# Kernel optimization log

Hardware: AMD Instinct MI355X
Metric: run time of the kernel (lower is better)

The kernel has to match this reference:

```python
import jax, jax.numpy as jnp
import numpy as np

B, S, H = 2, 2048, 1024
NH, HD = 16, 64
SCALE = HD ** -0.5


def setup_inputs() -> dict:
    key = jax.random.key(0)
    k1, k2, k3, k4 = jax.random.split(key, 4)
    hidden_states = jax.random.normal(k1, (B, S, H), dtype=jnp.float32)
    attention_mask = jax.random.randint(k2, (B, S), 0, 2, dtype=jnp.int32)
    # xavier-uniform-ish init scale
    w_qkv = jax.random.normal(k3, (3 * H, H), dtype=jnp.float32) * (2.0 / (H + 3 * H)) ** 0.5
    w_out = jax.random.normal(k4, (H, H), dtype=jnp.float32) * (1.0 / H) ** 0.5
    return {"hidden_states": hidden_states, "attention_mask": attention_mask,
            "w_qkv": w_qkv, "w_out": w_out}


def reference(hidden_states, attention_mask, w_qkv, w_out):
    b, s, _ = hidden_states.shape
    qkv = hidden_states @ w_qkv.T                      # [B,S,3H]
    q, k, v = jnp.split(qkv, 3, axis=-1)
    # [B,S,H] -> [B,NH,S,HD]
    reshape = lambda x: x.reshape(b, s, NH, HD).transpose(0, 2, 1, 3)
    q, k, v = reshape(q), reshape(k), reshape(v)
    scores = jnp.einsum('bhqd,bhkd->bhqk', q, k) * SCALE   # [B,NH,S,S]
    mask = attention_mask[:, None, None, :] == 0           # [B,1,1,S]
    scores = jnp.where(mask, -jnp.inf, scores)
    attn = jax.nn.softmax(scores, axis=-1)                 # dropout p: eval mode -> identity
    out = jnp.einsum('bhqk,bhkd->bhqd', attn, v)           # [B,NH,S,HD]
    out = out.transpose(0, 2, 1, 3).reshape(b, s, H)
    return out @ w_out.T
```

## Files before the change

kernel.cpp:

```cpp
#include <hip/hip_runtime.h>
#include <string.h>


typedef __bf16    bf16x8 __attribute__((ext_vector_type(8)));
typedef _Float16  f16x4  __attribute__((ext_vector_type(4)));
typedef _Float16  f16x2  __attribute__((ext_vector_type(2)));
typedef float     f32x4  __attribute__((ext_vector_type(4)));

#define NTOK   4096
#define HDIM   1024
#define SEQ    2048
#define NHEAD  16
#define F2SHIFT 4.0f
#define QSCALE  0.18033688f
#define LSTRIDE 68

__device__ __forceinline__ float bf2f(unsigned short u) {
    union { unsigned int i; float f; } x;
    x.i = ((unsigned int)u) << 16;
    return x.f;
}
__device__ __forceinline__ unsigned short f2bf(float f) {
    union { __bf16 h; unsigned short u; } x;
    x.h = (__bf16)f;
    return x.u;
}
__device__ __forceinline__ unsigned short f2h(float f) {
    union { _Float16 h; unsigned short u; } x;
    x.h = (_Float16)f;
    return x.u;
}
__device__ __forceinline__ f16x2 pkrtz(float a, float b) {
    union { __fp16 __attribute__((ext_vector_type(2))) i; f16x2 o; } x;
    x.i = __builtin_amdgcn_cvt_pkrtz(a, b);
    return x.o;
}

__device__ __forceinline__ int detect_f32(const unsigned short* hs) {
    unsigned int idx = (threadIdx.x & 63) * 4096u;
    float f = bf2f(hs[idx]);
    return __any(!(fabsf(f) < 1e4f));
}

typedef const __attribute__((address_space(1))) unsigned int* gptr_u32;
typedef __attribute__((address_space(3))) unsigned int* lptr_u32;

__device__ __forceinline__ void async16(const unsigned short* g, unsigned short* l) {
    __builtin_amdgcn_global_load_lds((gptr_u32)g, (lptr_u32)l, 16, 0, 0);
}

__global__ void convert3_kernel(const void* __restrict__ s0, const void* __restrict__ s1,
                                const void* __restrict__ s2, unsigned short* __restrict__ dst) {
    const int isf32 = detect_f32((const unsigned short*)s0);
    if (!isf32) return;
    int g = blockIdx.x * blockDim.x + threadIdx.x;
    const int stride = gridDim.x * blockDim.x;
    for (; g < 1048576; g += stride) {
        int i = g * 8;
        const void* src; int off;
        if (i < 4194304)      { src = s0; off = i; }
        else if (i < 7340032) { src = s1; off = i - 4194304; }
        else                  { src = s2; off = i - 7340032; }
        const float* s = (const float*)src + off;
        unsigned short o[8];
#pragma unroll
        for (int j = 0; j < 8; j++) o[j] = f2bf(s[j]);
        *(uint4*)(dst + i) = *(const uint4*)o;
    }
}

__global__ __launch_bounds__(256) void gemm_qkv(
    const unsigned short* __restrict__ Xc, const unsigned short* __restrict__ Wc,
    const unsigned short* __restrict__ Xraw, const unsigned short* __restrict__ Wraw,
    unsigned short* __restrict__ q_out, unsigned short* __restrict__ k_out,
    unsigned short* __restrict__ v_out) {
    const int K = 1024;
    __shared__ __align__(16) unsigned short Xs[128 * 32];
    __shared__ __align__(16) unsigned short Ws[128 * 32];

    const int isf32 = detect_f32(Xraw);
    const unsigned short* X = isf32 ? Xc : Xraw;
    const unsigned short* W = isf32 ? Wc : Wraw;

    const int t = threadIdx.x;
    const int w = t >> 6, lane = t & 63, quad = lane >> 4, lr = lane & 15;
    const int wrow = (w >> 1) * 64, wcol = (w & 1) * 64;
    const int m0 = blockIdx.y * 128, n0 = blockIdx.x * 128;
    const bool vblk = (n0 >= 2048);

    f32x4 acc[4][4];
#pragma unroll
    for (int mi = 0; mi < 4; mi++)
#pragma unroll
        for (int ni = 0; ni < 4; ni++) acc[mi][ni] = (f32x4){0.f, 0.f, 0.f, 0.f};

    const int srow = w * 32 + (lane >> 2);
    const int scol = (lane & 3) * 8;
    const unsigned short* xg = X + (size_t)(m0 + srow) * K + scol;
    const unsigned short* wg = W + (size_t)(n0 + srow) * K + scol;
    unsigned short* xl0 = &Xs[w * 1024];
    unsigned short* wl0 = &Ws[w * 1024];

    for (int k0 = 0; k0 < K; k0 += 32) {
        __syncthreads();
        async16(xg + k0, xl0);
        async16(xg + k0 + 16 * K, xl0 + 512);
        async16(wg + k0, wl0);
        async16(wg + k0 + 16 * K, wl0 + 512);
        __syncthreads();
        bf16x8 af[4], bfr[4];
#pragma unroll
        for (int mi = 0; mi < 4; mi++)
            af[mi] = *(bf16x8*)&Xs[(wrow + mi * 16 + lr) * 32 + quad * 8];
#pragma unroll
        for (int ni = 0; ni < 4; ni++)
            bfr[ni] = *(bf16x8*)&Ws[(wcol + ni * 16 + lr) * 32 + quad * 8];
        if (!vblk) {
#pragma unroll
            for (int mi = 0; mi < 4; mi++)
#pragma unroll
                for (int ni = 0; ni < 4; ni++)
                    acc[mi][ni] = __builtin_amdgcn_mfma_f32_16x16x32_bf16(af[mi], bfr[ni], acc[mi][ni], 0, 0, 0);
        } else {
#pragma unroll
            for (int mi = 0; mi < 4; mi++)
#pragma unroll
                for (int ni = 0; ni < 4; ni++)
                    acc[mi][ni] = __builtin_amdgcn_mfma_f32_16x16x32_bf16(bfr[ni], af[mi], acc[mi][ni], 0, 0, 0);
        }
    }

    if (!vblk) {
#pragma unroll
        for (int mi = 0; mi < 4; mi++)
#pragma unroll
            for (int ni = 0; ni < 4; ni++)
#pragma unroll
                for (int rr = 0; rr < 4; rr++) {
                    int mrow = m0 + wrow + mi * 16 + quad * 4 + rr;
                    int j = n0 + wcol + ni * 16 + lr;
                    float val = acc[mi][ni][rr];
                    int which = j >> 10, rem = j & 1023;
                    int nh = rem >> 6, hd = rem & 63;
                    int b = mrow >> 11, s = mrow & 2047;
                    size_t dst = ((size_t)(b * NHEAD + nh) * SEQ + s) * 64 + hd;
                    if (which == 0) q_out[dst] = f2bf(val * QSCALE);
                    else            k_out[dst] = f2bf(val);
                }
    } else {
#pragma unroll
        for (int mi = 0; mi < 4; mi++)
#pragma unroll
            for (int ni = 0; ni < 4; ni++)
#pragma unroll
                for (int rr = 0; rr < 4; rr++) {
                    int n = n0 + wcol + ni * 16 + quad * 4 + rr;
                    int m = m0 + wrow + mi * 16 + lr;
                    float val = acc[mi][ni][rr];
                    int rem = n & 1023;
                    int nh = rem >> 6, hd = rem & 63;
                    int b = m >> 11, s = m & 2047;
                    size_t dst = ((size_t)(b * NHEAD + nh) * 64 + hd) * SEQ + s;
                    v_out[dst] = f2h(val);
                }
    }
}

__global__ __launch_bounds__(256) void gemm_out(
    const unsigned short* __restrict__ X, const unsigned short* __restrict__ Wc,
    const unsigned short* __restrict__ Wraw,
    void* __restrict__ d_out, const unsigned short* __restrict__ hs_raw) {
    const int K = 1024, N = 1024;
    __shared__ __align__(16) unsigned short Xs[64 * 32];
    __shared__ __align__(16) unsigned short Ws[128 * 32];

    const int isf32 = detect_f32(hs_raw);
    const unsigned short* W = isf32 ? Wc : Wraw;

    const int t = threadIdx.x;
    const int w = t >> 6, lane = t & 63, quad = lane >> 4, lr = lane & 15;
    const int wrow = (w >> 1) * 32, wcol = (w & 1) * 64;
    const int m0 = blockIdx.y * 64, n0 = blockIdx.x * 128;

    f32x4 acc[2][4];
#pragma unroll
    for (int mi = 0; mi < 2; mi++)
#pragma unroll
        for (int ni = 0; ni < 4; ni++) acc[mi][ni] = (f32x4){0.f, 0.f, 0.f, 0.f};

    const int sxrow = w * 16 + (lane >> 2);
    const int swrow = w * 32 + (lane >> 2);
    const int scol = (lane & 3) * 8;
    const unsigned short* xg = X + (size_t)(m0 + sxrow) * K + scol;
    const unsigned short* wg = W + (size_t)(n0 + swrow) * K + scol;
    unsigned short* xl0 = &Xs[w * 512];
    unsigned short* wl0 = &Ws[w * 1024];

    for (int k0 = 0; k0 < K; k0 += 32) {
        __syncthreads();
        async16(xg + k0, xl0);
        async16(wg + k0, wl0);
        async16(wg + k0 + 16 * K, wl0 + 512);
        __syncthreads();
        bf16x8 af[2], bfr[4];
#pragma unroll
        for (int mi = 0; mi < 2; mi++)
            af[mi] = *(bf16x8*)&Xs[(wrow + mi * 16 + lr) * 32 + quad * 8];
#pragma unroll
        for (int ni = 0; ni < 4; ni++)
            bfr[ni] = *(bf16x8*)&Ws[(wcol + ni * 16 + lr) * 32 + quad * 8];
#pragma unroll
        for (int mi = 0; mi < 2; mi++)
#pragma unroll
            for (int ni = 0; ni < 4; ni++)
                acc[mi][ni] = __builtin_amdgcn_mfma_f32_16x16x32_bf16(af[mi], bfr[ni], acc[mi][ni], 0, 0, 0);
    }

#pragma unroll
    for (int mi = 0; mi < 2; mi++)
#pragma unroll
        for (int ni = 0; ni < 4; ni++)
#pragma unroll
            for (int rr = 0; rr < 4; rr++) {
                int mrow = m0 + wrow + mi * 16 + quad * 4 + rr;
                int j = n0 + wcol + ni * 16 + lr;
                float val = acc[mi][ni][rr];
                size_t dst = (size_t)mrow * N + j;
                if (isf32) ((float*)d_out)[dst] = val;
                else ((unsigned short*)d_out)[dst] = f2bf(val);
            }
}

__global__ __launch_bounds__(256) void flash_attn_v8(
    const unsigned short* __restrict__ q, const unsigned short* __restrict__ k,
    const unsigned short* __restrict__ vt, const int* __restrict__ mask,
    unsigned short* __restrict__ attn_out) {
    __shared__ __align__(16) unsigned short Ks[2][64 * LSTRIDE];
    __shared__ __align__(16) unsigned short Vt[2][64 * LSTRIDE];
    __shared__ __align__(16) float Msk[2][80];

    const int t = threadIdx.x;
    const int w = t >> 6, lane = t & 63, quad = lane >> 4, lr = lane & 15;
    const int bh = blockIdx.x, b = bh >> 4, h = bh & 15;
    const int q0 = blockIdx.y * 128;

    const unsigned short* qb = q + (size_t)bh * SEQ * 64;
    const unsigned short* kb = k + (size_t)bh * SEQ * 64;
    const unsigned short* vtb = vt + (size_t)bh * 64 * SEQ;
    const int* mb = mask + b * SEQ;

    bf16x8 qf[2][2];
#pragma unroll
    for (int qg = 0; qg < 2; qg++) {
        const unsigned short* qrow = qb + (size_t)(q0 + w * 32 + qg * 16 + lr) * 64 + quad * 8;
        qf[qg][0] = *(const bf16x8*)qrow;
        qf[qg][1] = *(const bf16x8*)(qrow + 32);
    }

    f32x4 oacc[2][4];
#pragma unroll
    for (int qg = 0; qg < 2; qg++)
#pragma unroll
        for (int dt = 0; dt < 4; dt++) oacc[qg][dt] = (f32x4){0.f, 0.f, 0.f, 0.f};
    float l_st[2] = {0.f, 0.f};

    const int sr = t >> 2;
    const int sc = (t & 3) * 16;

    uint4 ka, kb2, va, vb2;
    float mval = 0.f;
    {
        const uint4* kp = (const uint4*)(kb + (size_t)sr * 64 + sc);
        const uint4* vp = (const uint4*)(vtb + (size_t)sr * SEQ + sc);
        ka = kp[0]; kb2 = kp[1];
        va = vp[0]; vb2 = vp[1];
        if (t < 64) mval = (mb[t] == 0) ? -1e30f : -F2SHIFT;
    }
    *(uint4*)&Ks[0][sr * LSTRIDE + sc] = ka;
    *(uint4*)&Ks[0][sr * LSTRIDE + sc + 8] = kb2;
    *(uint4*)&Vt[0][sr * LSTRIDE + sc] = va;
    *(uint4*)&Vt[0][sr * LSTRIDE + sc + 8] = vb2;
    if (t < 64) Msk[0][t] = mval;
    __syncthreads();

    int cur = 0;
    for (int kk0 = 0; kk0 < SEQ; kk0 += 64) {
        const int nxt = kk0 + 64;
        if (nxt < SEQ) {
            const uint4* kp = (const uint4*)(kb + (size_t)(nxt + sr) * 64 + sc);
            const uint4* vp = (const uint4*)(vtb + (size_t)sr * SEQ + nxt + sc);
            ka = kp[0]; kb2 = kp[1];
            va = vp[0]; vb2 = vp[1];
            if (t < 64) mval = (mb[nxt + t] == 0) ? -1e30f : -F2SHIFT;
        }

        __builtin_amdgcn_s_setprio(1);
#pragma unroll
        for (int mt = 0; mt < 4; mt++) {
            bf16x8 a1h0 = *(bf16x8*)&Ks[cur][(mt * 16 + lr) * LSTRIDE + quad * 8];
            bf16x8 a1h1 = *(bf16x8*)&Ks[cur][(mt * 16 + lr) * LSTRIDE + 32 + quad * 8];
            f16x4 a2[4];
#pragma unroll
            for (int dt = 0; dt < 4; dt++)
                a2[dt] = *(f16x4*)&Vt[cur][(dt * 16 + lr) * LSTRIDE + mt * 16 + quad * 4];
            float4 mv = *(const float4*)&Msk[cur][mt * 16 + quad * 4];
            f32x4 zi = (f32x4){mv.x, mv.y, mv.z, mv.w};

#pragma unroll
            for (int qg = 0; qg < 2; qg++) {
                f32x4 z = __builtin_amdgcn_mfma_f32_16x16x32_bf16(a1h0, qf[qg][0], zi, 0, 0, 0);
                z = __builtin_amdgcn_mfma_f32_16x16x32_bf16(a1h1, qf[qg][1], z, 0, 0, 0);
                float p0 = __builtin_amdgcn_exp2f(z[0]);
                float p1 = __builtin_amdgcn_exp2f(z[1]);
                float p2 = __builtin_amdgcn_exp2f(z[2]);
                float p3 = __builtin_amdgcn_exp2f(z[3]);
                l_st[qg] += (p0 + p1) + (p2 + p3);
                f16x2 ab = pkrtz(p0, p1);
                f16x2 cd = pkrtz(p2, p3);
                f16x4 b2;
                b2[0] = ab[0]; b2[1] = ab[1]; b2[2] = cd[0]; b2[3] = cd[1];
#pragma unroll
                for (int dt = 0; dt < 4; dt++)
                    oacc[qg][dt] = __builtin_amdgcn_mfma_f32_16x16x16f16(a2[dt], b2, oacc[qg][dt], 0, 0, 0);
            }
        }
        __builtin_amdgcn_s_setprio(0);

        if (nxt < SEQ) {
            __syncthreads();
            const int nb = cur ^ 1;
            *(uint4*)&Ks[nb][sr * LSTRIDE + sc] = ka;
            *(uint4*)&Ks[nb][sr * LSTRIDE + sc + 8] = kb2;
            *(uint4*)&Vt[nb][sr * LSTRIDE + sc] = va;
            *(uint4*)&Vt[nb][sr * LSTRIDE + sc + 8] = vb2;
            if (t < 64) Msk[nb][t] = mval;
            __syncthreads();
            cur = nb;
        }
    }

    float inv[2];
#pragma unroll
    for (int qg = 0; qg < 2; qg++) {
        float s = l_st[qg];
        s += __shfl_xor(s, 16);
        s += __shfl_xor(s, 32);
        inv[qg] = 1.0f / s;
    }
#pragma unroll
    for (int qg = 0; qg < 2; qg++) {
        size_t tok = (size_t)(b * SEQ + q0 + w * 32 + qg * 16 + lr);
#pragma unroll
        for (int dt = 0; dt < 4; dt++)
#pragma unroll
            for (int rr = 0; rr < 4; rr++)
                attn_out[tok * HDIM + h * 64 + dt * 16 + quad * 4 + rr] =
                    f2bf(oacc[qg][dt][rr] * inv[qg]);
    }
}

extern "C" void kernel_launch(void* const* d_in, const int* in_sizes, int n_in,
                              void* d_out, int out_size, void* d_ws, size_t ws_size,
                              hipStream_t stream) {
    const void* hs_raw = d_in[0];
    const int* mask = (const int*)d_in[1];
    const void* wqkv_raw = d_in[2];
    const void* wout_raw = d_in[3];

    char* wsb = (char*)d_ws;
    unsigned short* hs_c = (unsigned short*)(wsb + 256);
    unsigned short* wqkv_c = hs_c + 4194304;
    unsigned short* wout_c = wqkv_c + 3145728;
    unsigned short* qw = wout_c + 1048576;
    unsigned short* kw = qw + 4194304;
    unsigned short* vtw = kw + 4194304;
    unsigned short* ao = vtw + 4194304;

    convert3_kernel<<<1024, 256, 0, stream>>>(hs_raw, wqkv_raw, wout_raw, hs_c);

    gemm_qkv<<<dim3(24, 32), 256, 0, stream>>>(hs_c, wqkv_c,
                                               (const unsigned short*)hs_raw,
                                               (const unsigned short*)wqkv_raw,
                                               qw, kw, vtw);
    flash_attn_v8<<<dim3(32, 16), 256, 0, stream>>>(qw, kw, vtw, mask, ao);
    gemm_out<<<dim3(8, 64), 256, 0, stream>>>(ao, wout_c,
                                              (const unsigned short*)wout_raw, d_out,
                                              (const unsigned short*)hs_raw);
}
```

Measured before the change: 202.6 us.

## Split attention KV range across two warp groups per block and merge partials

The flash attention kernel now uses 512 threads, with two groups of 4 waves each covering half of the key sequence for the same 128 queries. Each group keeps its own double-buffered K/V/mask tiles in shared memory. At the end, group 1 writes its partial output accumulators and row sums to shared memory and group 0 adds them before normalising. This is meant to double the waves per block, adding latency hiding and parallelism for a grid of only 512 blocks. In exchange it doubles shared memory per block and adds a cross-group reduction. The merge adds partials directly, which is valid because the softmax uses a fixed shift rather than a running max.

New measurement: 207.3 us. 2.3% more time.

```diff
diff --git a/kernel.cpp b/kernel.cpp
--- a/kernel.cpp
+++ b/kernel.cpp
@@ -14,6 +14,7 @@
 #define F2SHIFT 4.0f
 #define QSCALE  0.18033688f
 #define LSTRIDE 68
+#define KHALF  1024
 
 __device__ __forceinline__ float bf2f(unsigned short u) {
     union { unsigned int i; float f; } x;
@@ -231,18 +232,21 @@
             }
 }
 
-__global__ __launch_bounds__(256) void flash_attn_v8(
+__global__ __launch_bounds__(512) void flash_attn_v9(
     const unsigned short* __restrict__ q, const unsigned short* __restrict__ k,
     const unsigned short* __restrict__ vt, const int* __restrict__ mask,
     unsigned short* __restrict__ attn_out) {
-    __shared__ __align__(16) unsigned short Ks[2][64 * LSTRIDE];
-    __shared__ __align__(16) unsigned short Vt[2][64 * LSTRIDE];
-    __shared__ __align__(16) float Msk[2][80];
+    __shared__ __align__(16) unsigned short Ks[2][2][64 * LSTRIDE];
+    __shared__ __align__(16) unsigned short Vt[2][2][64 * LSTRIDE];
+    __shared__ __align__(16) float Msk[2][2][80];
 
     const int t = threadIdx.x;
-    const int w = t >> 6, lane = t & 63, quad = lane >> 4, lr = lane & 15;
+    const int g = t >> 8;
+    const int tt = t & 255;
+    const int wl = tt >> 6, lane = t & 63, quad = lane >> 4, lr = lane & 15;
     const int bh = blockIdx.x, b = bh >> 4, h = bh & 15;
     const int q0 = blockIdx.y * 128;
+    const int kbase = g * KHALF;
 
     const unsigned short* qb = q + (size_t)bh * SEQ * 64;
     const unsigned short* kb = k + (size_t)bh * SEQ * 64;
@@ -252,7 +256,7 @@
     bf16x8 qf[2][2];
 #pragma unroll
     for (int qg = 0; qg < 2; qg++) {
-        const unsigned short* qrow = qb + (size_t)(q0 + w * 32 + qg * 16 + lr) * 64 + quad * 8;
+        const unsigned short* qrow = qb + (size_t)(q0 + wl * 32 + qg * 16 + lr) * 64 + quad * 8;
         qf[qg][0] = *(const bf16x8*)qrow;
         qf[qg][1] = *(const bf16x8*)(qrow + 32);
     }
@@ -264,46 +268,46 @@
         for (int dt = 0; dt < 4; dt++) oacc[qg][dt] = (f32x4){0.f, 0.f, 0.f, 0.f};
     float l_st[2] = {0.f, 0.f};
 
-    const int sr = t >> 2;
-    const int sc = (t & 3) * 16;
+    const int sr = tt >> 2;
+    const int sc = (tt & 3) * 16;
 
     uint4 ka, kb2, va, vb2;
     float mval = 0.f;
     {
-        const uint4* kp = (const uint4*)(kb + (size_t)sr * 64 + sc);
-        const uint4* vp = (const uint4*)(vtb + (size_t)sr * SEQ + sc);
+        const uint4* kp = (const uint4*)(kb + (size_t)(kbase + sr) * 64 + sc);
+        const uint4* vp = (const uint4*)(vtb + (size_t)sr * SEQ + kbase + sc);
         ka = kp[0]; kb2 = kp[1];
         va = vp[0]; vb2 = vp[1];
-        if (t < 64) mval = (mb[t] == 0) ? -1e30f : -F2SHIFT;
-    }
-    *(uint4*)&Ks[0][sr * LSTRIDE + sc] = ka;
-    *(uint4*)&Ks[0][sr * LSTRIDE + sc + 8] = kb2;
-    *(uint4*)&Vt[0][sr * LSTRIDE + sc] = va;
-    *(uint4*)&Vt[0][sr * LSTRIDE + sc + 8] = vb2;
-    if (t < 64) Msk[0][t] = mval;
+        if (tt < 64) mval = (mb[kbase + tt] == 0) ? -1e30f : -F2SHIFT;
+    }
+    *(uint4*)&Ks[g][0][sr * LSTRIDE + sc] = ka;
+    *(uint4*)&Ks[g][0][sr * LSTRIDE + sc + 8] = kb2;
+    *(uint4*)&Vt[g][0][sr * LSTRIDE + sc] = va;
+    *(uint4*)&Vt[g][0][sr * LSTRIDE + sc + 8] = vb2;
+    if (tt < 64) Msk[g][0][tt] = mval;
     __syncthreads();
 
     int cur = 0;
-    for (int kk0 = 0; kk0 < SEQ; kk0 += 64) {
+    for (int kk0 = 0; kk0 < KHALF; kk0 += 64) {
         const int nxt = kk0 + 64;
-        if (nxt < SEQ) {
-            const uint4* kp = (const uint4*)(kb + (size_t)(nxt + sr) * 64 + sc);
-            const uint4* vp = (const uint4*)(vtb + (size_t)sr * SEQ + nxt + sc);
+        if (nxt < KHALF) {
+            const uint4* kp = (const uint4*)(kb + (size_t)(kbase + nxt + sr) * 64 + sc);
+            const uint4* vp = (const uint4*)(vtb + (size_t)sr * SEQ + kbase + nxt + sc);
             ka = kp[0]; kb2 = kp[1];
             va = vp[0]; vb2 = vp[1];
-            if (t < 64) mval = (mb[nxt + t] == 0) ? -1e30f : -F2SHIFT;
+            if (tt < 64) mval = (mb[kbase + nxt + tt] == 0) ? -1e30f : -F2SHIFT;
         }
 
         __builtin_amdgcn_s_setprio(1);
 #pragma unroll
         for (int mt = 0; mt < 4; mt++) {
-            bf16x8 a1h0 = *(bf16x8*)&Ks[cur][(mt * 16 + lr) * LSTRIDE + quad * 8];
-            bf16x8 a1h1 = *(bf16x8*)&Ks[cur][(mt * 16 + lr) * LSTRIDE + 32 + quad * 8];
+            bf16x8 a1h0 = *(bf16x8*)&Ks[g][cur][(mt * 16 + lr) * LSTRIDE + quad * 8];
+            bf16x8 a1h1 = *(bf16x8*)&Ks[g][cur][(mt * 16 + lr) * LSTRIDE + 32 + quad * 8];
             f16x4 a2[4];
 #pragma unroll
             for (int dt = 0; dt < 4; dt++)
-                a2[dt] = *(f16x4*)&Vt[cur][(dt * 16 + lr) * LSTRIDE + mt * 16 + quad * 4];
-            float4 mv = *(const float4*)&Msk[cur][mt * 16 + quad * 4];
+                a2[dt] = *(f16x4*)&Vt[g][cur][(dt * 16 + lr) * LSTRIDE + mt * 16 + quad * 4];
+            float4 mv = *(const float4*)&Msk[g][cur][mt * 16 + quad * 4];
             f32x4 zi = (f32x4){mv.x, mv.y, mv.z, mv.w};
 
 #pragma unroll
@@ -326,36 +330,57 @@
         }
         __builtin_amdgcn_s_setprio(0);
 
-        if (nxt < SEQ) {
+        if (nxt < KHALF) {
             __syncthreads();
             const int nb = cur ^ 1;
-            *(uint4*)&Ks[nb][sr * LSTRIDE + sc] = ka;
-            *(uint4*)&Ks[nb][sr * LSTRIDE + sc + 8] = kb2;
-            *(uint4*)&Vt[nb][sr * LSTRIDE + sc] = va;
-            *(uint4*)&Vt[nb][sr * LSTRIDE + sc + 8] = vb2;
-            if (t < 64) Msk[nb][t] = mval;
+            *(uint4*)&Ks[g][nb][sr * LSTRIDE + sc] = ka;
+            *(uint4*)&Ks[g][nb][sr * LSTRIDE + sc + 8] = kb2;
+            *(uint4*)&Vt[g][nb][sr * LSTRIDE + sc] = va;
+            *(uint4*)&Vt[g][nb][sr * LSTRIDE + sc + 8] = vb2;
+            if (tt < 64) Msk[g][nb][tt] = mval;
             __syncthreads();
             cur = nb;
         }
     }
 
-    float inv[2];
+    float lsum[2];
 #pragma unroll
     for (int qg = 0; qg < 2; qg++) {
         float s = l_st[qg];
         s += __shfl_xor(s, 16);
         s += __shfl_xor(s, 32);
-        inv[qg] = 1.0f / s;
-    }
-#pragma unroll
-    for (int qg = 0; qg < 2; qg++) {
-        size_t tok = (size_t)(b * SEQ + q0 + w * 32 + qg * 16 + lr);
-#pragma unroll
-        for (int dt = 0; dt < 4; dt++)
-#pragma unroll
-            for (int rr = 0; rr < 4; rr++)
-                attn_out[tok * HDIM + h * 64 + dt * 16 + quad * 4 + rr] =
-                    f2bf(oacc[qg][dt][rr] * inv[qg]);
+        lsum[qg] = s;
+    }
+
+    float* Oex = (float*)&Ks[0][0][0];
+    float* Lex = (float*)&Vt[0][0][0];
+    __syncthreads();
+    if (g == 1) {
+#pragma unroll
+        for (int qg = 0; qg < 2; qg++) {
+            const int r = (wl * 2 + qg) * 16 + lr;
+            if (quad == 0) Lex[r] = lsum[qg];
+#pragma unroll
+            for (int dt = 0; dt < 4; dt++)
+                *(f32x4*)&Oex[r * 68 + dt * 16 + quad * 4] = oacc[qg][dt];
+        }
+    }
+    __syncthreads();
+    if (g == 0) {
+#pragma unroll
+        for (int qg = 0; qg < 2; qg++) {
+            const int r = (wl * 2 + qg) * 16 + lr;
+            const float inv = 1.0f / (lsum[qg] + Lex[r]);
+            size_t tok = (size_t)(b * SEQ + q0 + wl * 32 + qg * 16 + lr);
+#pragma unroll
+            for (int dt = 0; dt < 4; dt++) {
+                f32x4 op = *(f32x4*)&Oex[r * 68 + dt * 16 + quad * 4];
+#pragma unroll
+                for (int rr = 0; rr < 4; rr++)
+                    attn_out[tok * HDIM + h * 64 + dt * 16 + quad * 4 + rr] =
+                        f2bf((oacc[qg][dt][rr] + op[rr]) * inv);
+            }
+        }
     }
 }
 
@@ -382,7 +407,7 @@
                                                (const unsigned short*)hs_raw,
                                                (const unsigned short*)wqkv_raw,
                                                qw, kw, vtw);
-    flash_attn_v8<<<dim3(32, 16), 256, 0, stream>>>(qw, kw, vtw, mask, ao);
+    flash_attn_v9<<<dim3(32, 16), 512, 0, stream>>>(qw, kw, vtw, mask, ao);
     gemm_out<<<dim3(8, 64), 256, 0, stream>>>(ao, wout_c,
                                               (const unsigned short*)wout_raw, d_out,
                                               (const unsigned short*)hs_raw);
```

## Split attention over two key halves with a separate combine kernel

Applied to the files above, without the earlier changes.

The flash attention grid gains a z dimension of two, so each block handles half of the key sequence. Each block writes unnormalized fp16 partial outputs and row sums into reused workspace buffers. A new combine kernel adds the two partials, normalizes them and writes bf16. This doubles the block count from 512, which should fill the GPU better, at the cost of an extra launch, extra global traffic for the partials, and fp16 range risk on the unnormalized sums.

Result: slower. 208.9 us (+3.1%).

```diff
diff --git a/kernel.cpp b/kernel.cpp
--- a/kernel.cpp
+++ b/kernel.cpp
@@ -3,6 +3,7 @@
 
 
 typedef __bf16    bf16x8 __attribute__((ext_vector_type(8)));
+typedef _Float16  f16x8  __attribute__((ext_vector_type(8)));
 typedef _Float16  f16x4  __attribute__((ext_vector_type(4)));
 typedef _Float16  f16x2  __attribute__((ext_vector_type(2)));
 typedef float     f32x4  __attribute__((ext_vector_type(4)));
@@ -14,6 +15,7 @@
 #define F2SHIFT 4.0f
 #define QSCALE  0.18033688f
 #define LSTRIDE 68
+#define KHALF  1024
 
 __device__ __forceinline__ float bf2f(unsigned short u) {
     union { unsigned int i; float f; } x;
@@ -231,10 +233,11 @@
             }
 }
 
-__global__ __launch_bounds__(256) void flash_attn_v8(
+__global__ __launch_bounds__(256) void flash_attn_v10(
     const unsigned short* __restrict__ q, const unsigned short* __restrict__ k,
     const unsigned short* __restrict__ vt, const int* __restrict__ mask,
-    unsigned short* __restrict__ attn_out) {
+    unsigned short* __restrict__ o0, unsigned short* __restrict__ o1,
+    float* __restrict__ lbuf) {
     __shared__ __align__(16) unsigned short Ks[2][64 * LSTRIDE];
     __shared__ __align__(16) unsigned short Vt[2][64 * LSTRIDE];
     __shared__ __align__(16) float Msk[2][80];
@@ -243,6 +246,8 @@
     const int w = t >> 6, lane = t & 63, quad = lane >> 4, lr = lane & 15;
     const int bh = blockIdx.x, b = bh >> 4, h = bh & 15;
     const int q0 = blockIdx.y * 128;
+    const int kslice = blockIdx.z;
+    const int kbase = kslice * KHALF;
 
     const unsigned short* qb = q + (size_t)bh * SEQ * 64;
     const unsigned short* kb = k + (size_t)bh * SEQ * 64;
@@ -270,11 +275,11 @@
     uint4 ka, kb2, va, vb2;
     float mval = 0.f;
     {
-        const uint4* kp = (const uint4*)(kb + (size_t)sr * 64 + sc);
-        const uint4* vp = (const uint4*)(vtb + (size_t)sr * SEQ + sc);
+        const uint4* kp = (const uint4*)(kb + (size_t)(kbase + sr) * 64 + sc);
+        const uint4* vp = (const uint4*)(vtb + (size_t)sr * SEQ + kbase + sc);
         ka = kp[0]; kb2 = kp[1];
         va = vp[0]; vb2 = vp[1];
-        if (t < 64) mval = (mb[t] == 0) ? -1e30f : -F2SHIFT;
+        if (t < 64) mval = (mb[kbase + t] == 0) ? -1e30f : -F2SHIFT;
     }
     *(uint4*)&Ks[0][sr * LSTRIDE + sc] = ka;
     *(uint4*)&Ks[0][sr * LSTRIDE + sc + 8] = kb2;
@@ -284,14 +289,14 @@
     __syncthreads();
 
     int cur = 0;
-    for (int kk0 = 0; kk0 < SEQ; kk0 += 64) {
+    for (int kk0 = 0; kk0 < KHALF; kk0 += 64) {
         const int nxt = kk0 + 64;
-        if (nxt < SEQ) {
-            const uint4* kp = (const uint4*)(kb + (size_t)(nxt + sr) * 64 + sc);
-            const uint4* vp = (const uint4*)(vtb + (size_t)sr * SEQ + nxt + sc);
+        if (nxt < KHALF) {
+            const uint4* kp = (const uint4*)(kb + (size_t)(kbase + nxt + sr) * 64 + sc);
+            const uint4* vp = (const uint4*)(vtb + (size_t)sr * SEQ + kbase + nxt + sc);
             ka = kp[0]; kb2 = kp[1];
             va = vp[0]; vb2 = vp[1];
-            if (t < 64) mval = (mb[nxt + t] == 0) ? -1e30f : -F2SHIFT;
+            if (t < 64) mval = (mb[kbase + nxt + t] == 0) ? -1e30f : -F2SHIFT;
         }
 
         __builtin_amdgcn_s_setprio(1);
@@ -326,7 +331,7 @@
         }
         __builtin_amdgcn_s_setprio(0);
 
-        if (nxt < SEQ) {
+        if (nxt < KHALF) {
             __syncthreads();
             const int nb = cur ^ 1;
             *(uint4*)&Ks[nb][sr * LSTRIDE + sc] = ka;
@@ -339,24 +344,40 @@
         }
     }
 
-    float inv[2];
+    unsigned short* od = kslice ? o1 : o0;
 #pragma unroll
     for (int qg = 0; qg < 2; qg++) {
         float s = l_st[qg];
         s += __shfl_xor(s, 16);
         s += __shfl_xor(s, 32);
-        inv[qg] = 1.0f / s;
-    }
-#pragma unroll
-    for (int qg = 0; qg < 2; qg++) {
-        size_t tok = (size_t)(b * SEQ + q0 + w * 32 + qg * 16 + lr);
+        const int qrow = q0 + w * 32 + qg * 16 + lr;
+        if (quad == 0) lbuf[kslice * 65536 + bh * 2048 + qrow] = s;
+        size_t tok = (size_t)(b * SEQ + qrow);
 #pragma unroll
         for (int dt = 0; dt < 4; dt++)
 #pragma unroll
             for (int rr = 0; rr < 4; rr++)
-                attn_out[tok * HDIM + h * 64 + dt * 16 + quad * 4 + rr] =
-                    f2bf(oacc[qg][dt][rr] * inv[qg]);
-    }
+                od[tok * HDIM + h * 64 + dt * 16 + quad * 4 + rr] =
+                    f2h(oacc[qg][dt][rr]);
+    }
+}
+
+__global__ __launch_bounds__(256) void combine_kernel(
+    unsigned short* __restrict__ o0,
+    const unsigned short* __restrict__ o1,
+    const float* __restrict__ lbuf) {
+    const int g = blockIdx.x * blockDim.x + threadIdx.x;
+    const int i = g * 8;
+    const int tok = i >> 10, col = i & 1023;
+    const int b = tok >> 11, s = tok & 2047, h = col >> 6;
+    const int li = (b * 16 + h) * 2048 + s;
+    const float inv = 1.0f / (lbuf[li] + lbuf[65536 + li]);
+    f16x8 a = *(const f16x8*)(o0 + i);
+    f16x8 bb = *(const f16x8*)(o1 + i);
+    unsigned short ov[8];
+#pragma unroll
+    for (int j = 0; j < 8; j++) ov[j] = f2bf(((float)a[j] + (float)bb[j]) * inv);
+    *(uint4*)(o0 + i) = *(const uint4*)ov;
 }
 
 extern "C" void kernel_launch(void* const* d_in, const int* in_sizes, int n_in,
@@ -376,13 +397,17 @@
     unsigned short* vtw = kw + 4194304;
     unsigned short* ao = vtw + 4194304;
 
+    unsigned short* o1 = hs_c;
+    float* lbuf = (float*)wqkv_c;
+
     convert3_kernel<<<1024, 256, 0, stream>>>(hs_raw, wqkv_raw, wout_raw, hs_c);
 
     gemm_qkv<<<dim3(24, 32), 256, 0, stream>>>(hs_c, wqkv_c,
                                                (const unsigned short*)hs_raw,
                                                (const unsigned short*)wqkv_raw,
                                                qw, kw, vtw);
-    flash_attn_v8<<<dim3(32, 16), 256, 0, stream>>>(qw, kw, vtw, mask, ao);
+    flash_attn_v10<<<dim3(32, 16, 2), 256, 0, stream>>>(qw, kw, vtw, mask, ao, o1, lbuf);
+    combine_kernel<<<2048, 256, 0, stream>>>(ao, o1, lbuf);
     gemm_out<<<dim3(8, 64), 256, 0, stream>>>(ao, wout_c,
                                               (const unsigned short*)wout_raw, d_out,
                                               (const unsigned short*)hs_raw);
```
